# Kernel tuning notes

Measured on AMD Instinct MI355X. Metric: run time of the kernel, lower is better.

## Reference

```python
import jax, jax.numpy as jnp
import numpy as np

GX, GY, GZ = 128, 128, 32
D = 64
N = 100000
MIN_B = jnp.array([-20.0, -20.0, -2.0], jnp.float32)
MAX_B = jnp.array([20.0, 20.0, 6.0], jnp.float32)
GRID = jnp.array([GX, GY, GZ], jnp.float32)
VOX = (MAX_B - MIN_B) / GRID  # voxel sizes per axis
ELL = 0.5
SIGMA = 1.0
PI = float(np.pi)
EPS = 1e-6


def sparse_kernel(d):
    v = SIGMA * ((1.0 / 3.0) * (2.0 + jnp.cos(2.0 * PI * d / ELL)) * (1.0 - d / ELL)
                 + (1.0 / (2.0 * PI)) * jnp.sin(2.0 * PI * d / ELL))
    v = jnp.where(d >= ELL, 0.0, v)
    return jnp.clip(v, 0.0, 1.0)


def setup_inputs() -> dict:
    key = jax.random.key(0)
    k1, k2, k3, k4 = jax.random.split(key, 4)
    mean_map = jax.random.normal(k1, (GX, GY, GZ, D), jnp.float32) * 0.1
    variance_map = jnp.ones((GX, GY, GZ, D), jnp.float32)
    confidence_map = jax.random.uniform(k2, (GX, GY, GZ, 1), jnp.float32) * 2.0
    xyz = jax.random.uniform(k3, (N, 3), jnp.float32) * (MAX_B - MIN_B) + MIN_B
    feat = jax.random.normal(k4, (N, D), jnp.float32)
    point_cloud = jnp.concatenate([xyz, feat], axis=-1)  # (N, 3+D)
    return {"mean_map": mean_map, "variance_map": variance_map,
            "confidence_map": confidence_map, "point_cloud": point_cloud}


def reference(mean_map, variance_map, confidence_map, point_cloud):
    xyz = point_cloud[:, :3]
    feat = point_cloud[:, 3:]  # (N, D) latent features
    grid_inds = jnp.floor((xyz - MIN_B) / VOX)  # (N,3) float voxel indices

    # 27 neighbor offsets (filter_size=3)
    r = jnp.arange(-1, 2)
    offs = jnp.stack(jnp.meshgrid(r, r, r, indexing='ij'), axis=-1).reshape(-1, 3)  # (27,3)
    nb = grid_inds[:, None, :] + offs[None].astype(grid_inds.dtype)  # (N,27,3)
    valid = jnp.all((nb >= 0.0) & (nb < GRID), axis=-1)  # (N,27)

    # pseudo-discrete distance: neighbor centroid minus point's voxel centroid
    dvec = (nb * VOX + MIN_B) - (grid_inds * VOX + MIN_B)[:, None, :]  # (N,27,3)
    d = jnp.linalg.norm(dvec, axis=-1, keepdims=True)  # (N,27,1)
    kval = sparse_kernel(d) * valid[..., None].astype(d.dtype)  # zero out invalid

    G = GX * GY * GZ
    nb_i = jnp.clip(nb.astype(jnp.int32), 0, jnp.array([GX - 1, GY - 1, GZ - 1], jnp.int32))
    lin = ((nb_i[..., 0] * GY + nb_i[..., 1]) * GZ + nb_i[..., 2]).reshape(-1)  # (N*27,)
    kf = kval.reshape(-1, 1)  # (N*27,1)
    ff = jnp.broadcast_to(feat[:, None, :], (feat.shape[0], 27, D)).reshape(-1, D)

    k_bar = jax.ops.segment_sum(kf, lin, num_segments=G)            # (G,1)
    y_sum = jax.ops.segment_sum(kf * ff, lin, num_segments=G)       # (G,D)
    y_bar = y_sum / (k_bar + EPS)
    delta = ff - y_bar[lin]                                          # (N*27,D)
    S_bar = jax.ops.segment_sum(kf * delta * delta, lin, num_segments=G)

    k_bar = k_bar.reshape(GX, GY, GZ, 1)
    y_bar = y_bar.reshape(GX, GY, GZ, D)
    S_bar = S_bar.reshape(GX, GY, GZ, D)

    # variance update (uses pre-update mean/confidence); zero at untouched voxels
    delta_mean = y_bar - mean_map
    scaling = confidence_map * k_bar / (confidence_map + k_bar + EPS)
    new_variance = variance_map + S_bar + scaling * delta_mean * delta_mean
    new_mean = (confidence_map * mean_map + k_bar * y_bar) / (confidence_map + k_bar + EPS)
    new_confidence = confidence_map + k_bar
    return new_mean, new_variance, new_confidence
```

## Files before the change

kernel.cpp:

```cpp
#include <hip/hip_runtime.h>
#include <math.h>

#define GXD 128
#define GYD 128
#define GZD 32
#define DD  64
#define GCELLS (GXD * GYD * GZD)

#define MINX (-20.0f)
#define MINY (-20.0f)
#define MINZ (-2.0f)
#define VOXX (0.3125f)
#define VOXY (0.3125f)
#define VOXZ (0.25f)
#define ELL  (0.5f)
#define EPSV (1e-6f)
#define PIF  (3.14159265358979323846f)

typedef float v2f __attribute__((ext_vector_type(2)));
typedef float v4f __attribute__((ext_vector_type(4)));

struct KvCols { float w0[9]; float w1[9]; };
#define IS_PLUS(c) ((c) == 1 || (c) == 3 || (c) == 4 || (c) == 5 || (c) == 7)

__device__ __forceinline__ float kval_of(int o) {
    int ox = o / 9 - 1;
    int oy = (o / 3) % 3 - 1;
    int oz = o % 3 - 1;
    float dx = ox * VOXX, dy = oy * VOXY, dz = oz * VOXZ;
    float d = sqrtf(dx * dx + dy * dy + dz * dz);
    float ang = 2.0f * PIF * d / ELL;
    float v = (1.0f / 3.0f) * (2.0f + cosf(ang)) * (1.0f - d / ELL)
            + (1.0f / (2.0f * PIF)) * sinf(ang);
    v = (d >= ELL) ? 0.0f : v;
    return fminf(fmaxf(v, 0.0f), 1.0f);
}

__device__ __forceinline__ int base_cell(const float* __restrict__ row,
                                         int* cx, int* cy, int* cz) {
    float x = row[0], y = row[1], z = row[2];
    int gx = (int)floorf((x - MINX) / VOXX);
    int gy = (int)floorf((y - MINY) / VOXY);
    int gz = (int)floorf((z - MINZ) / VOXZ);
    gx = min(max(gx, 0), GXD - 1);
    gy = min(max(gy, 0), GYD - 1);
    gz = min(max(gz, 0), GZD - 1);
    *cx = gx; *cy = gy; *cz = gz;
    return (gx * GYD + gy) * GZD + gz;
}


__global__ void lbki_zero_rows(const float* __restrict__ pc,
                               float2* __restrict__ MM2,
                               int npts) {
    int lane = threadIdx.x & 63;
    int wave = threadIdx.x >> 6;
    int p = blockIdx.x * (blockDim.x >> 6) + wave;
    if (p >= npts) return;
    int cx, cy, cz;
    int g = base_cell(pc + (size_t)p * 67, &cx, &cy, &cz);
    MM2[(size_t)g * DD + lane]       = make_float2(0.0f, 0.0f);
    MM2[(size_t)(g ^ 1) * DD + lane] = make_float2(0.0f, 0.0f);
}

__global__ void lbki_build(const float* __restrict__ pc,
                           float* __restrict__ M0,
                           float* __restrict__ MM,
                           int npts) {
    int lane = threadIdx.x & 63;
    int wave = threadIdx.x >> 6;
    int p = blockIdx.x * (blockDim.x >> 6) + wave;
    if (p >= npts) return;
    const float* row = pc + (size_t)p * 67;
    int cx, cy, cz;
    int g = base_cell(row, &cx, &cy, &cz);
    float f = row[3 + lane];
    size_t e = ((size_t)g * DD + lane) * 2;
    atomicAdd(&MM[e],     f);
    atomicAdd(&MM[e + 1], f * f);
    if (lane == 0) atomicAdd(&M0[g], 1.0f);
}

__global__ __launch_bounds__(512)
void lbki_stencil_colC(const float* __restrict__ M0,
                       const float* __restrict__ MM,
                       const float* __restrict__ mean_map,
                       const float* __restrict__ var_map,
                       const float* __restrict__ conf_map,
                       float* __restrict__ out_mean,
                       float* __restrict__ out_var,
                       float* __restrict__ out_conf,
                       KvCols ka) {
    __shared__ v4f      smPairs[2 * 30 * 64];
    __shared__ float    sm0[3 * 10 * 35];
    __shared__ float    kb_lds[256];
    __shared__ unsigned smask[30];
    const int tid  = threadIdx.x;
    const int lane = tid & 63;
    const int wave = __builtin_amdgcn_readfirstlane(tid >> 6);
    const int half = lane >> 5;
    const int l5   = lane & 31;

    unsigned bid = blockIdx.x;
    unsigned chunk = gridDim.x >> 3;
    unsigned swz = (bid & 7u) * chunk + (bid >> 3);
    const int col0 = (int)(swz * 8u);
    const int cx  = col0 >> 7;
    const int cy0 = col0 & 127;

    for (int e = tid; e < 3 * 10 * 35; e += 512) {
        int xo = e / 350;
        int r  = e - xo * 350;
        int yo = r / 35;
        int zp = r - yo * 35;
        int z  = zp - 1;
        int gx_ = cx - 1 + xo;
        int gy_ = cy0 - 1 + yo;
        bool v = ((unsigned)gx_ < (unsigned)GXD) &&
                 ((unsigned)gy_ < (unsigned)GYD) && ((unsigned)z < (unsigned)GZD);
        float val = 0.0f;
        if (v) val = M0[((gx_ << 7) + gy_) * 32 + z];
        sm0[e] = val;
    }
    __syncthreads();

    if (tid < 256) {
        int j = tid >> 5, z = tid & 31;
        float kb = 0.0f;
        #pragma unroll
        for (int c = 0; c < 9; ++c) {
            const float* sc = sm0 + ((c / 3) * 10 + j + c % 3) * 35 + z + 1;
            kb += ka.w0[c] * sc[0];
            if (IS_PLUS(c)) kb += ka.w1[c] * (sc[-1] + sc[1]);
        }
        kb_lds[(j << 5) + z] = kb;
        unsigned cell = (unsigned)((cx << 7) + cy0 + j) * 32u + (unsigned)z;
        out_conf[cell] = conf_map[cell] + kb;
    } else if (tid < 256 + 30) {
        int idx = tid - 256;
        const float* sc = sm0 + idx * 35 + 1;
        unsigned m = 0;
        for (int z = 0; z < 32; ++z)
            if (sc[z] != 0.0f) m |= (1u << z);
        smask[idx] = m;
    }
    __syncthreads();

    const int cy = cy0 + wave;
    const char* sentp = (const char*)MM + (size_t)GCELLS * 512u;

    unsigned mkO[3]; const char* tpO[3];
    #pragma unroll
    for (int x = 0; x < 3; ++x) {
        mkO[x] = (unsigned)__builtin_amdgcn_readfirstlane(
                     (int)smask[x * 10 + wave + 1]);
        int nx = cx + x - 1;
        bool v = ((unsigned)nx < (unsigned)GXD);
        tpO[x] = v ? ((const char*)MM + (size_t)(((nx << 7) + cy) << 5) * 512u)
                   : sentp;
    }
    const bool haloW = (wave == 0) || (wave == 7);
    const int  hyo   = (wave == 0) ? 0 : 9;
    const int  hy    = cy0 - 1 + hyo;
    unsigned mkH[3]; const char* tpH[3];
    #pragma unroll
    for (int x = 0; x < 3; ++x) {
        mkH[x] = (unsigned)__builtin_amdgcn_readfirstlane(
                     (int)smask[x * 10 + hyo]);
        int nx = cx + x - 1;
        bool v = ((unsigned)nx < (unsigned)GXD) && ((unsigned)hy < (unsigned)GYD);
        tpH[x] = v ? ((const char*)MM + (size_t)(((nx << 7) + hy) << 5) * 512u)
                   : sentp;
    }
    const int laneB = lane * 16;

    v4f* tapBase = &smPairs[(wave) * 64 + lane];
    v4f* wrBase  = &smPairs[(wave + 1) * 64 + lane];
    v4f* hwBase  = &smPairs[hyo * 64 + lane];

    const unsigned gbase = (unsigned)((cx << 7) + cy) * 32u;
    const int rowB  = (int)(gbase * 256u) + l5 * 8;
    const int mapsB = rowB - half * 256;
    const unsigned gb = gbase * 4u;

    const char* MEc = (const char*)mean_map;
    const char* VAc = (const char*)var_map;
    const char* COc = (const char*)conf_map;
    char*       OMc = (char*)out_mean;
    char*       OVc = (char*)out_var;
    const float* kbp = kb_lds + (wave << 5);

    v4f inf[9];
    v4f H = (v4f)0.0f, Hp = (v4f)0.0f, recv = (v4f)0.0f, Rp = (v4f)0.0f;
    v4f rA[3], rH[3];
    rH[0] = rH[1] = rH[2] = (v4f)0.0f;
    v2f mb[2], vb[2];
    float cb[2];

#define REDUCE(T0, T1)                                                  \
    v4f T0 = (v4f)0.0f, T1 = (v4f)0.0f;                                 \
    _Pragma("unroll")                                                   \
    for (int c = 0; c < 9; ++c) {                                       \
        T0 += inf[c] * ka.w0[c];                                        \
        if (IS_PLUS(c)) T1 += inf[c] * ka.w1[c];                        \
    }

#define SWAP32(DST, SRC)                                                \
    DST.x = __shfl_xor(SRC.x, 32, 64);                                  \
    DST.y = __shfl_xor(SRC.y, 32, 64);                                  \
    DST.z = __shfl_xor(SRC.z, 32, 64);                                  \
    DST.w = __shfl_xor(SRC.w, 32, 64);

#define FINSTORE(W, KB, MB, VB, CB, ADDR)                               \
    {                                                                   \
        float kb_  = (KB);                                              \
        float cf_  = (CB);                                              \
        float rin  = __builtin_amdgcn_rcpf(kb_ + EPSV);                 \
        float rden = __builtin_amdgcn_rcpf(cf_ + kb_ + EPSV);           \
        float scal = cf_ * kb_ * rden;                                  \
        float ya = (W).x * rin, yb = (W).z * rin;                       \
        float Sa = (W).y - 2.0f * ya * (W).x + ya * ya * kb_;           \
        float Sb = (W).w - 2.0f * yb * (W).z + yb * yb * kb_;           \
        float da = ya - (MB).x, db = yb - (MB).y;                       \
        v2f om, ov;                                                     \
        om.x = (cf_ * (MB).x + kb_ * ya) * rden;                        \
        om.y = (cf_ * (MB).y + kb_ * yb) * rden;                        \
        ov.x = (VB).x + Sa + scal * da * da;                            \
        ov.y = (VB).y + Sb + scal * db * db;                            \
        __builtin_nontemporal_store(om, (v2f*)(OMc + (ADDR)));          \
        __builtin_nontemporal_store(ov, (v2f*)(OVc + (ADDR)));          \
    }

#define TAPS_READ(BUF)                                                  \
    _Pragma("unroll")                                                   \
    for (int c = 0; c < 9; ++c)                                         \
        inf[c] = tapBase[(BUF) * 1920 + ((c / 3) * 10 + (c % 3)) * 64];

#define STAGE_ISSUE(SHIFT, TOFF)                                        \
    _Pragma("unroll")                                                   \
    for (int x = 0; x < 3; ++x) {                                       \
        const char* p_ = ((mkO[x] >> (SHIFT)) & 3u) ? tpO[x] : sentp;   \
        rA[x] = *(const v4f*)(p_ + laneB + (TOFF) * 1024);              \
    }                                                                   \
    if (haloW) {                                                        \
        _Pragma("unroll")                                               \
        for (int x = 0; x < 3; ++x) {                                   \
            const char* p_ = ((mkH[x] >> (SHIFT)) & 3u) ? tpH[x] : sentp; \
            rH[x] = *(const v4f*)(p_ + laneB + (TOFF) * 1024);          \
        }                                                               \
    }

#define STAGE_WRITE(BUF)                                                \
    _Pragma("unroll")                                                   \
    for (int x = 0; x < 3; ++x)                                         \
        wrBase[(BUF) * 1920 + x * 640] = rA[x];                         \
    if (haloW) {                                                        \
        _Pragma("unroll")                                               \
        for (int x = 0; x < 3; ++x)                                     \
            hwBase[(BUF) * 1920 + x * 640] = rH[x];                     \
    }

#define BARRIER                                                         \
    asm volatile("s_waitcnt lgkmcnt(0)" ::: "memory");                  \
    __builtin_amdgcn_s_barrier();                                       \
    asm volatile("" ::: "memory");

    STAGE_ISSUE(0, 0)
    STAGE_WRITE(0)
    STAGE_ISSUE(2, 1)
    mb[0] = __builtin_nontemporal_load((const v2f*)(MEc + rowB));
    vb[0] = __builtin_nontemporal_load((const v2f*)(VAc + rowB));
    cb[0] = *(const float*)(COc + gb);
    mb[1] = __builtin_nontemporal_load((const v2f*)(MEc + mapsB + 512));
    vb[1] = __builtin_nontemporal_load((const v2f*)(VAc + mapsB + 512));
    cb[1] = *(const float*)(COc + gb + 8 - half * 4);
    BARRIER

    {
        TAPS_READ(0)
        REDUCE(t0, t1)
        STAGE_WRITE(1)
        STAGE_ISSUE(4, 2)
        SWAP32(recv, t1)
        H = t0 + recv;
        if (!half) {
            FINSTORE(H, kbp[0], mb[0], vb[0], cb[0], rowB)
        }
        Hp = H; Rp = recv;
        mb[0] = __builtin_nontemporal_load((const v2f*)(MEc + mapsB + 1024));
        vb[0] = __builtin_nontemporal_load((const v2f*)(VAc + mapsB + 1024));
        cb[0] = *(const float*)(COc + gb + 16 - half * 4);
        BARRIER
    }

    #pragma unroll
    for (int t = 1; t <= 15; ++t) {
        TAPS_READ(t & 1)
        REDUCE(t0, t1)
        if (t < 15) {
            STAGE_WRITE((t + 1) & 1)
            if (t < 14) {
                STAGE_ISSUE(2 * t + 4, t + 2)
            }
        }
        SWAP32(recv, t1)
        H = t0 + recv;
        v4f finv = half ? (Hp + recv) : (H + Rp);
        float kbv = kbp[2 * t - half];
        FINSTORE(finv, kbv, mb[t & 1], vb[t & 1], cb[t & 1], mapsB + t * 512)
        Hp = H; Rp = recv;
        if (t < 15) {
            mb[(t + 1) & 1] = __builtin_nontemporal_load((const v2f*)(MEc + mapsB + (t + 1) * 512));
            vb[(t + 1) & 1] = __builtin_nontemporal_load((const v2f*)(VAc + mapsB + (t + 1) * 512));
            cb[(t + 1) & 1] = *(const float*)(COc + gb + (t + 1) * 8 - half * 4);
            BARRIER
        } else {
            int a16 = min(mapsB + 16 * 512, rowB + 31 * 256);
            mb[0] = __builtin_nontemporal_load((const v2f*)(MEc + a16));
            vb[0] = __builtin_nontemporal_load((const v2f*)(VAc + a16));
            cb[0] = *(const float*)(COc + min(gb + 128u - (unsigned)(half * 4), gb + 124u));
        }
    }

    if (half) {
        FINSTORE(Hp, kbp[31], mb[0], vb[0], cb[0], mapsB + 16 * 512)
    }
#undef BARRIER
#undef STAGE_WRITE
#undef STAGE_ISSUE
#undef TAPS_READ
#undef FINSTORE
#undef SWAP32
#undef REDUCE
}

__global__ void lbki_accum(const float* __restrict__ pc,
                           float* __restrict__ y_sum,
                           float* __restrict__ sq_sum,
                           float* __restrict__ k_bar,
                           int npts) {
    __shared__ float kval_s[27];
    if (threadIdx.x < 27) kval_s[threadIdx.x] = kval_of(threadIdx.x);
    __syncthreads();

    int lane = threadIdx.x & 63;
    int wave = threadIdx.x >> 6;
    int p = blockIdx.x * (blockDim.x >> 6) + wave;
    if (p >= npts) return;

    const float* row = pc + (size_t)p * 67;
    int gx, gy, gz;
    base_cell(row, &gx, &gy, &gz);
    float f = row[3 + lane];
    float ff = f * f;

    #pragma unroll
    for (int o = 0; o < 27; ++o) {
        float kv = kval_s[o];
        if (kv <= 0.0f) continue;
        int nx = gx + (o / 9) - 1;
        int ny = gy + ((o / 3) % 3) - 1;
        int nz = gz + (o % 3) - 1;
        if ((unsigned)nx >= (unsigned)GXD) continue;
        if ((unsigned)ny >= (unsigned)GYD) continue;
        if ((unsigned)nz >= (unsigned)GZD) continue;
        size_t g = ((size_t)nx * GYD + ny) * GZD + nz;
        atomicAdd(&y_sum[g * DD + lane], kv * f);
        atomicAdd(&sq_sum[g * DD + lane], kv * ff);
        if (lane == 0) atomicAdd(&k_bar[g], kv);
    }
}

__global__ void lbki_finalize(const float* __restrict__ mean_map,
                              const float* __restrict__ var_map,
                              const float* __restrict__ conf_map,
                              float* __restrict__ out_mean,
                              float* __restrict__ out_var,
                              float* __restrict__ out_conf) {
    int lane = threadIdx.x & 63;
    int wave = threadIdx.x >> 6;
    int g = blockIdx.x * (blockDim.x >> 6) + wave;
    if (g >= GCELLS) return;

    float kb   = out_conf[g];
    float conf = conf_map[g];

    size_t idx = (size_t)g * DD + lane;
    float ys   = out_mean[idx];
    float sq   = out_var[idx];
    float mean = mean_map[idx];
    float var  = var_map[idx];

    float ybar  = ys / (kb + EPSV);
    float Sbar  = sq - 2.0f * ybar * ys + ybar * ybar * kb;
    float denom = conf + kb + EPSV;
    float dm    = ybar - mean;
    float scal  = conf * kb / denom;

    out_mean[idx] = (conf * mean + kb * ybar) / denom;
    out_var[idx]  = var + Sbar + scal * dm * dm;
    if (lane == 0) out_conf[g] = conf + kb;
}

extern "C" void kernel_launch(void* const* d_in, const int* in_sizes, int n_in,
                              void* d_out, int out_size, void* d_ws, size_t ws_size,
                              hipStream_t stream) {
    const float* mean_map = (const float*)d_in[0];
    const float* var_map  = (const float*)d_in[1];
    const float* conf_map = (const float*)d_in[2];
    const float* pc       = (const float*)d_in[3];
    int npts = in_sizes[3] / 67;

    float* out      = (float*)d_out;
    float* out_mean = out;
    float* out_var  = out + (size_t)GCELLS * DD;
    float* out_conf = out + (size_t)2 * GCELLS * DD;

    const size_t M0_ELEMS = (size_t)GCELLS;
    const size_t MM_ELEMS = (size_t)GCELLS * 128 + 8192;
    const size_t WS_NEEDED = (M0_ELEMS + MM_ELEMS) * sizeof(float);

    if (ws_size >= WS_NEEDED) {
        float* M0 = (float*)d_ws;
        float* MM = M0 + M0_ELEMS;

        hipMemsetAsync(M0, 0, M0_ELEMS * sizeof(float), stream);
        hipMemsetAsync(MM + (size_t)GCELLS * 128, 0, 8192 * sizeof(float), stream);

        int wpb = 4;
        int pblocks = (npts + wpb - 1) / wpb;
        lbki_zero_rows<<<pblocks, 256, 0, stream>>>(pc, (float2*)MM, npts);
        lbki_build<<<pblocks, 256, 0, stream>>>(pc, M0, MM, npts);

        KvCols ka;
        for (int c = 0; c < 9; ++c) {
            int ox = c / 3 - 1, oy = c % 3 - 1;
            for (int k = 0; k < 2; ++k) {
                double dx = ox * (double)VOXX;
                double dy = oy * (double)VOXY;
                double dz = k  * (double)VOXZ;
                double d  = sqrt(dx * dx + dy * dy + dz * dz);
                double ang = 2.0 * (double)PIF * d / (double)ELL;
                double v = (1.0 / 3.0) * (2.0 + cos(ang)) * (1.0 - d / (double)ELL)
                         + (1.0 / (2.0 * (double)PIF)) * sin(ang);
                if (d >= (double)ELL) v = 0.0;
                v = v < 0.0 ? 0.0 : (v > 1.0 ? 1.0 : v);
                if (k == 0) ka.w0[c] = (float)v; else ka.w1[c] = (float)v;
            }
        }

        int sblocks = (GXD * GYD) / 8;
        lbki_stencil_colC<<<sblocks, 512, 0, stream>>>(M0, MM,
                                                       mean_map, var_map, conf_map,
                                                       out_mean, out_var, out_conf,
                                                       ka);
    } else {
        hipMemsetAsync(d_out, 0, (size_t)out_size * sizeof(float), stream);
        int wpb = 4;
        int blocks = (npts + wpb - 1) / wpb;
        lbki_accum<<<blocks, 256, 0, stream>>>(pc, out_mean, out_var, out_conf, npts);
        int fblocks = GCELLS / 4;
        lbki_finalize<<<fblocks, 256, 0, stream>>>(mean_map, var_map, conf_map,
                                                   out_mean, out_var, out_conf);
    }
}
```

Before: 272.5 us.

## Spread halo loads across six waves and mask untouched cells at LDS write

The halo-row loads that waves 0 and 7 each issued three at a time are now split across waves 1-6, each issuing one load, which balances per-wave memory traffic. Cells never touched by a point no longer need zeroed neighbour rows: the occupancy mask selects zero when writing taps into LDS. This allows dropping the second zeroing store in the zero-rows kernel, the sentinel buffer and its memset. The cost is extra select logic per staged write, and correctness now depends on the mask bits matching the half-lane cell layout.

```diff
diff --git a/kernel.cpp b/kernel.cpp
--- a/kernel.cpp
+++ b/kernel.cpp
@@ -59,8 +59,7 @@
     if (p >= npts) return;
     int cx, cy, cz;
     int g = base_cell(pc + (size_t)p * 67, &cx, &cy, &cz);
-    MM2[(size_t)g * DD + lane]       = make_float2(0.0f, 0.0f);
-    MM2[(size_t)(g ^ 1) * DD + lane] = make_float2(0.0f, 0.0f);
+    MM2[(size_t)g * DD + lane] = make_float2(0.0f, 0.0f);
 }
 
 __global__ void lbki_build(const float* __restrict__ pc,
@@ -82,7 +81,7 @@
 }
 
 __global__ __launch_bounds__(512)
-void lbki_stencil_colC(const float* __restrict__ M0,
+void lbki_stencil_colD(const float* __restrict__ M0,
                        const float* __restrict__ MM,
                        const float* __restrict__ mean_map,
                        const float* __restrict__ var_map,
@@ -147,7 +146,7 @@
     __syncthreads();
 
     const int cy = cy0 + wave;
-    const char* sentp = (const char*)MM + (size_t)GCELLS * 512u;
+    const char* sentp = (const char*)MM;
 
     unsigned mkO[3]; const char* tpO[3];
     #pragma unroll
@@ -159,24 +158,24 @@
         tpO[x] = v ? ((const char*)MM + (size_t)(((nx << 7) + cy) << 5) * 512u)
                    : sentp;
     }
-    const bool haloW = (wave == 0) || (wave == 7);
-    const int  hyo   = (wave == 0) ? 0 : 9;
-    const int  hy    = cy0 - 1 + hyo;
-    unsigned mkH[3]; const char* tpH[3];
-    #pragma unroll
-    for (int x = 0; x < 3; ++x) {
-        mkH[x] = (unsigned)__builtin_amdgcn_readfirstlane(
-                     (int)smask[x * 10 + hyo]);
-        int nx = cx + x - 1;
-        bool v = ((unsigned)nx < (unsigned)GXD) && ((unsigned)hy < (unsigned)GYD);
-        tpH[x] = v ? ((const char*)MM + (size_t)(((nx << 7) + hy) << 5) * 512u)
-                   : sentp;
-    }
+    const bool haloW = (wave >= 1) && (wave <= 6);
+    const int combo  = haloW ? (wave - 1) : 0;
+    const int hx     = combo % 3;
+    const int hyo    = (combo / 3) ? 9 : 0;
+    const int hy     = cy0 - 1 + hyo;
+    unsigned mkH = (unsigned)__builtin_amdgcn_readfirstlane(
+                       (int)smask[hx * 10 + hyo]);
+    int hnx = cx + hx - 1;
+    bool hv = ((unsigned)hnx < (unsigned)GXD) && ((unsigned)hy < (unsigned)GYD);
+    const char* tpH = hv ? ((const char*)MM +
+                            (size_t)(((hnx << 7) + hy) << 5) * 512u)
+                         : sentp;
+
     const int laneB = lane * 16;
 
     v4f* tapBase = &smPairs[(wave) * 64 + lane];
     v4f* wrBase  = &smPairs[(wave + 1) * 64 + lane];
-    v4f* hwBase  = &smPairs[hyo * 64 + lane];
+    v4f* hwPtr   = &smPairs[(hx * 10 + hyo) * 64 + lane];
 
     const unsigned gbase = (unsigned)((cx << 7) + cy) * 32u;
     const int rowB  = (int)(gbase * 256u) + l5 * 8;
@@ -192,8 +191,8 @@
 
     v4f inf[9];
     v4f H = (v4f)0.0f, Hp = (v4f)0.0f, recv = (v4f)0.0f, Rp = (v4f)0.0f;
-    v4f rA[3], rH[3];
-    rH[0] = rH[1] = rH[2] = (v4f)0.0f;
+    v4f rA[3], rH;
+    rH = (v4f)0.0f;
     v2f mb[2], vb[2];
     float cb[2];
 
@@ -243,21 +242,21 @@
         rA[x] = *(const v4f*)(p_ + laneB + (TOFF) * 1024);              \
     }                                                                   \
     if (haloW) {                                                        \
-        _Pragma("unroll")                                               \
-        for (int x = 0; x < 3; ++x) {                                   \
-            const char* p_ = ((mkH[x] >> (SHIFT)) & 3u) ? tpH[x] : sentp; \
-            rH[x] = *(const v4f*)(p_ + laneB + (TOFF) * 1024);          \
-        }                                                               \
-    }
-
-#define STAGE_WRITE(BUF)                                                \
+        const char* p_ = ((mkH >> (SHIFT)) & 3u) ? tpH : sentp;         \
+        rH = *(const v4f*)(p_ + laneB + (TOFF) * 1024);                 \
+    }
+
+#define STAGE_WRITE(BUF, SH)                                            \
     _Pragma("unroll")                                                   \
-    for (int x = 0; x < 3; ++x)                                         \
-        wrBase[(BUF) * 1920 + x * 640] = rA[x];                         \
+    for (int x = 0; x < 3; ++x) {                                       \
+        unsigned b_ = (mkO[x] >> (SH)) & 3u;                            \
+        bool keep_ = (half ? (b_ & 2u) : (b_ & 1u)) != 0u;              \
+        wrBase[(BUF) * 1920 + x * 640] = keep_ ? rA[x] : (v4f)0.0f;     \
+    }                                                                   \
     if (haloW) {                                                        \
-        _Pragma("unroll")                                               \
-        for (int x = 0; x < 3; ++x)                                     \
-            hwBase[(BUF) * 1920 + x * 640] = rH[x];                     \
+        unsigned b_ = (mkH >> (SH)) & 3u;                               \
+        bool keep_ = (half ? (b_ & 2u) : (b_ & 1u)) != 0u;              \
+        hwPtr[(BUF) * 1920] = keep_ ? rH : (v4f)0.0f;                   \
     }
 
 #define BARRIER                                                         \
@@ -266,7 +265,7 @@
     asm volatile("" ::: "memory");
 
     STAGE_ISSUE(0, 0)
-    STAGE_WRITE(0)
+    STAGE_WRITE(0, 0)
     STAGE_ISSUE(2, 1)
     mb[0] = __builtin_nontemporal_load((const v2f*)(MEc + rowB));
     vb[0] = __builtin_nontemporal_load((const v2f*)(VAc + rowB));
@@ -279,7 +278,7 @@
     {
         TAPS_READ(0)
         REDUCE(t0, t1)
-        STAGE_WRITE(1)
+        STAGE_WRITE(1, 2)
         STAGE_ISSUE(4, 2)
         SWAP32(recv, t1)
         H = t0 + recv;
@@ -298,7 +297,7 @@
         TAPS_READ(t & 1)
         REDUCE(t0, t1)
         if (t < 15) {
-            STAGE_WRITE((t + 1) & 1)
+            STAGE_WRITE((t + 1) & 1, 2 * t + 2)
             if (t < 14) {
                 STAGE_ISSUE(2 * t + 4, t + 2)
             }
@@ -417,7 +416,7 @@
     float* out_conf = out + (size_t)2 * GCELLS * DD;
 
     const size_t M0_ELEMS = (size_t)GCELLS;
-    const size_t MM_ELEMS = (size_t)GCELLS * 128 + 8192;
+    const size_t MM_ELEMS = (size_t)GCELLS * 128;
     const size_t WS_NEEDED = (M0_ELEMS + MM_ELEMS) * sizeof(float);
 
     if (ws_size >= WS_NEEDED) {
@@ -425,7 +424,6 @@
         float* MM = M0 + M0_ELEMS;
 
         hipMemsetAsync(M0, 0, M0_ELEMS * sizeof(float), stream);
-        hipMemsetAsync(MM + (size_t)GCELLS * 128, 0, 8192 * sizeof(float), stream);
 
         int wpb = 4;
         int pblocks = (npts + wpb - 1) / wpb;
@@ -450,7 +448,7 @@
         }
 
         int sblocks = (GXD * GYD) / 8;
-        lbki_stencil_colC<<<sblocks, 512, 0, stream>>>(M0, MM,
+        lbki_stencil_colD<<<sblocks, 512, 0, stream>>>(M0, MM,
                                                        mean_map, var_map, conf_map,
                                                        out_mean, out_var, out_conf,
                                                        ka);
```

After: 258.0 us, median of 2. -5.3%, faster.

## Single-buffer stencil LDS staging with extra barrier; merge sentinel memset

Applied to the files above, without the earlier changes.

Halves the shared-memory pair staging buffer from double to single buffering. Each step now reads its taps, synchronizes, and then overwrites the buffer before the reduction runs. This is meant to cut LDS footprint so more blocks fit per CU. The cost is an additional barrier per z-step and less overlap between LDS writes and compute. The zero sentinel region moves in front of MM, so a single memset covers both M0 and the sentinel.

```diff
diff --git a/kernel.cpp b/kernel.cpp
--- a/kernel.cpp
+++ b/kernel.cpp
@@ -82,7 +82,7 @@
 }
 
 __global__ __launch_bounds__(512)
-void lbki_stencil_colC(const float* __restrict__ M0,
+void lbki_stencil_colE(const float* __restrict__ M0,
                        const float* __restrict__ MM,
                        const float* __restrict__ mean_map,
                        const float* __restrict__ var_map,
@@ -91,7 +91,7 @@
                        float* __restrict__ out_var,
                        float* __restrict__ out_conf,
                        KvCols ka) {
-    __shared__ v4f      smPairs[2 * 30 * 64];
+    __shared__ v4f      smPairs[30 * 64];
     __shared__ float    sm0[3 * 10 * 35];
     __shared__ float    kb_lds[256];
     __shared__ unsigned smask[30];
@@ -147,7 +147,7 @@
     __syncthreads();
 
     const int cy = cy0 + wave;
-    const char* sentp = (const char*)MM + (size_t)GCELLS * 512u;
+    const char* sentp = (const char*)MM - 32768;
 
     unsigned mkO[3]; const char* tpO[3];
     #pragma unroll
@@ -231,10 +231,10 @@
         __builtin_nontemporal_store(ov, (v2f*)(OVc + (ADDR)));          \
     }
 
-#define TAPS_READ(BUF)                                                  \
+#define TAPS_READ                                                       \
     _Pragma("unroll")                                                   \
     for (int c = 0; c < 9; ++c)                                         \
-        inf[c] = tapBase[(BUF) * 1920 + ((c / 3) * 10 + (c % 3)) * 64];
+        inf[c] = tapBase[((c / 3) * 10 + (c % 3)) * 64];
 
 #define STAGE_ISSUE(SHIFT, TOFF)                                        \
     _Pragma("unroll")                                                   \
@@ -250,14 +250,14 @@
         }                                                               \
     }
 
-#define STAGE_WRITE(BUF)                                                \
+#define STAGE_WRITE                                                     \
     _Pragma("unroll")                                                   \
     for (int x = 0; x < 3; ++x)                                         \
-        wrBase[(BUF) * 1920 + x * 640] = rA[x];                         \
+        wrBase[x * 640] = rA[x];                                        \
     if (haloW) {                                                        \
         _Pragma("unroll")                                               \
         for (int x = 0; x < 3; ++x)                                     \
-            hwBase[(BUF) * 1920 + x * 640] = rH[x];                     \
+            hwBase[x * 640] = rH[x];                                    \
     }
 
 #define BARRIER                                                         \
@@ -266,7 +266,7 @@
     asm volatile("" ::: "memory");
 
     STAGE_ISSUE(0, 0)
-    STAGE_WRITE(0)
+    STAGE_WRITE
     STAGE_ISSUE(2, 1)
     mb[0] = __builtin_nontemporal_load((const v2f*)(MEc + rowB));
     vb[0] = __builtin_nontemporal_load((const v2f*)(VAc + rowB));
@@ -277,10 +277,11 @@
     BARRIER
 
     {
-        TAPS_READ(0)
+        TAPS_READ
+        BARRIER
+        STAGE_WRITE
+        STAGE_ISSUE(4, 2)
         REDUCE(t0, t1)
-        STAGE_WRITE(1)
-        STAGE_ISSUE(4, 2)
         SWAP32(recv, t1)
         H = t0 + recv;
         if (!half) {
@@ -295,14 +296,15 @@
 
     #pragma unroll
     for (int t = 1; t <= 15; ++t) {
-        TAPS_READ(t & 1)
-        REDUCE(t0, t1)
+        TAPS_READ
         if (t < 15) {
-            STAGE_WRITE((t + 1) & 1)
+            BARRIER
+            STAGE_WRITE
             if (t < 14) {
                 STAGE_ISSUE(2 * t + 4, t + 2)
             }
         }
+        REDUCE(t0, t1)
         SWAP32(recv, t1)
         H = t0 + recv;
         v4f finv = half ? (Hp + recv) : (H + Rp);
@@ -416,16 +418,16 @@
     float* out_var  = out + (size_t)GCELLS * DD;
     float* out_conf = out + (size_t)2 * GCELLS * DD;
 
-    const size_t M0_ELEMS = (size_t)GCELLS;
-    const size_t MM_ELEMS = (size_t)GCELLS * 128 + 8192;
-    const size_t WS_NEEDED = (M0_ELEMS + MM_ELEMS) * sizeof(float);
+    const size_t M0_ELEMS   = (size_t)GCELLS;
+    const size_t SENT_ELEMS = 8192;
+    const size_t MM_ELEMS   = (size_t)GCELLS * 128;
+    const size_t WS_NEEDED  = (M0_ELEMS + SENT_ELEMS + MM_ELEMS) * sizeof(float);
 
     if (ws_size >= WS_NEEDED) {
         float* M0 = (float*)d_ws;
-        float* MM = M0 + M0_ELEMS;
-
-        hipMemsetAsync(M0, 0, M0_ELEMS * sizeof(float), stream);
-        hipMemsetAsync(MM + (size_t)GCELLS * 128, 0, 8192 * sizeof(float), stream);
+        float* MM = M0 + M0_ELEMS + SENT_ELEMS;
+
+        hipMemsetAsync(M0, 0, (M0_ELEMS + SENT_ELEMS) * sizeof(float), stream);
 
         int wpb = 4;
         int pblocks = (npts + wpb - 1) / wpb;
@@ -450,7 +452,7 @@
         }
 
         int sblocks = (GXD * GYD) / 8;
-        lbki_stencil_colC<<<sblocks, 512, 0, stream>>>(M0, MM,
+        lbki_stencil_colE<<<sblocks, 512, 0, stream>>>(M0, MM,
                                                        mean_map, var_map, conf_map,
                                                        out_mean, out_var, out_conf,
                                                        ka);
```

After: 280.0 us. 2.8% more time.
